# Kernel tuning notes

Hardware: AMD Instinct MI355X
Metric: run time of the kernel (lower is better)

Reference implementation:

```python
import jax, jax.numpy as jnp
import numpy as np

N, D_IN, D_OUT = 8192, 1024, 1024

def setup_inputs() -> dict:
    key = jax.random.key(0)
    k0, k1, k2, k3 = jax.random.split(key, 4)
    scale = 1.0 / np.sqrt(D_IN)
    return {
        "inputs": jax.random.normal(k0, (N, D_IN), dtype=jnp.float32),
        "W_q": jax.random.uniform(k1, (D_IN, D_OUT), jnp.float32, -scale, scale),
        "W_k": jax.random.uniform(k2, (D_IN, D_OUT), jnp.float32, -scale, scale),
        "W_v": jax.random.uniform(k3, (D_IN, D_OUT), jnp.float32, -scale, scale),
    }

def reference(inputs, W_q, W_k, W_v):
    # Linear projections (no bias): [N, d_out]
    q = inputs @ W_q
    k = inputs @ W_k
    v = inputs @ W_v
    d_k = k.shape[-1]
    # Full N x N scores, scaled softmax over last axis
    scores = (q @ k.T) / jnp.sqrt(jnp.asarray(d_k, q.dtype))
    attn = jax.nn.softmax(scores, axis=-1)
    return attn @ v
```

## Files before the change

kernel.cpp:

```cpp
#include <hip/hip_runtime.h>
#include <hip/hip_fp16.h>
#include <stdint.h>


typedef _Float16 half_t;
typedef _Float16 half8 __attribute__((ext_vector_type(8)));
typedef _Float16 half4 __attribute__((ext_vector_type(4)));
typedef float f32x4 __attribute__((ext_vector_type(4)));
typedef int i32x4 __attribute__((ext_vector_type(4)));

#define GLOAD16(gp, lp)                                                        \
  __builtin_amdgcn_global_load_lds(                                            \
      (__attribute__((address_space(1))) void*)(gp),                           \
      (__attribute__((address_space(3))) void*)(lp), 16, 0, 0)

#define BAR() __builtin_amdgcn_s_barrier()
#define LGKM0() asm volatile("s_waitcnt lgkmcnt(0)")
#define VMCNT8() asm volatile("s_waitcnt vmcnt(8)")
#define VMCNT4() asm volatile("s_waitcnt vmcnt(4)")
#define VMCNT0() asm volatile("s_waitcnt vmcnt(0)")

__global__ __launch_bounds__(256) void cast_f32_to_f16(
    const float* __restrict__ in, half_t* __restrict__ out, int n4) {
  int i = blockIdx.x * 256 + threadIdx.x;
  if (i < n4) {
    float4 v = ((const float4*)in)[i];
    half4 o = {(half_t)v.x, (half_t)v.y, (half_t)v.z, (half_t)v.w};
    ((half4*)out)[i] = o;
  }
}

template <typename Tin>
__global__ __launch_bounds__(256) void transpose_cast(
    const Tin* __restrict__ in, int ldin, half_t* __restrict__ out, int ldout,
    int R, int C) {
  __shared__ half_t tile[64][65];
  const int c0 = blockIdx.x * 64, r0 = blockIdx.y * 64;
  const int tx = threadIdx.x & 63, ty = threadIdx.x >> 6;
#pragma unroll
  for (int i = 0; i < 16; i++) {
    int r = ty * 16 + i;
    tile[r][tx] = (half_t)in[(size_t)(r0 + r) * ldin + c0 + tx];
  }
  __syncthreads();
#pragma unroll
  for (int i = 0; i < 16; i++) {
    int c = ty * 16 + i;
    out[(size_t)(c0 + c) * ldout + r0 + tx] = tile[tx][c];
  }
}

__global__ __launch_bounds__(256) void quant_i8(
    const half_t* __restrict__ in, int ldin, int8_t* __restrict__ out,
    int ldout, int n8) {
  int i = blockIdx.x * 256 + threadIdx.x;
  if (i >= n8) return;
  int row = i >> 7;
  int g = (i & 127) * 8;
  half8 v = *(const half8*)(in + (size_t)row * ldin + g);
  int b[8];
#pragma unroll
  for (int j = 0; j < 8; j++) {
    float f = (float)v[j] * 32.f;
    f = fminf(fmaxf(f, -127.f), 127.f);
    b[j] = (int)rintf(f);
  }
  int lo = (b[0] & 255) | ((b[1] & 255) << 8) | ((b[2] & 255) << 16) |
           ((b[3] & 255) << 24);
  int hi = (b[4] & 255) | ((b[5] & 255) << 8) | ((b[6] & 255) << 16) |
           ((b[7] & 255) << 24);
  int2* p = (int2*)(out + (size_t)row * ldout + g);
  *p = make_int2(lo, hi);
}

__global__ __launch_bounds__(256) void rowsum_recip(
    const float* __restrict__ rowpart, float* __restrict__ rinv, int rows,
    int w4) {
  int r = blockIdx.x * 256 + threadIdx.x;
  if (r < rows) {
    const float4* p = (const float4*)(rowpart + (size_t)r * (w4 * 4));
    float s = 0.f;
    for (int i = 0; i < w4; i++) {
      float4 v = p[i];
      s += v.x + v.y + v.z + v.w;
    }
    rinv[r] = 1.f / s;
  }
}

__global__ __launch_bounds__(256) void reduce_add2_norm(
    const float4* __restrict__ a, const float4* __restrict__ b,
    const float* __restrict__ rinv, float4* __restrict__ o, int n) {
  int i = blockIdx.x * 256 + threadIdx.x;
  if (i < n) {
    float4 x = a[i], y = b[i];
    float s = rinv[i >> 8];
    x.x = (x.x + y.x) * s;
    x.y = (x.y + y.y) * s;
    x.z = (x.z + y.z) * s;
    x.w = (x.w + y.w) * s;
    o[i] = x;
  }
}

template <typename To, int MODE>
__global__ __launch_bounds__(512, 2) void gemm256(
    const half_t* __restrict__ A, int lda, const half_t* __restrict__ Bt,
    int ldb, To* __restrict__ C, int ldc, int M, int N, int K, int ychunks,
    int SG, float* __restrict__ rowpart) {
  __shared__ __align__(16) char sm[131072];

  const int t = threadIdx.x;
  const int w = t >> 6;
  const int ln = t & 63;

  const int nwg = gridDim.x * gridDim.y;
  const int bid = blockIdx.y * gridDim.x + blockIdx.x;
  const int cpx = nwg >> 3;
  const int q = (bid & 7) * cpx + (bid >> 3);
  const int tiles_y = gridDim.y / ychunks;
  const int per_chunk = gridDim.x * tiles_y;
  const int chunk = q / per_chunk;
  int r_ = q - chunk * per_chunk;
  const int sw = SG * tiles_y;
  const int s_ = r_ / sw;
  r_ -= s_ * sw;
  const int by = r_ / SG;
  const int bx = s_ * SG + (r_ - by * SG);

  A += (size_t)chunk * K;
  Bt += (size_t)chunk * K;
  C += (size_t)chunk * M * ldc;

  const int row0 = by * 256;
  const int col0 = bx * 256;

  const int srow = w * 8 + (ln >> 3);
  const int sslot = (ln & 7) ^ ((ln >> 3) & 7);
  const half_t* Ag = A + (size_t)(row0 + srow) * lda + sslot * 8;
  const half_t* Bg = Bt + (size_t)(col0 + srow) * ldb + sslot * 8;
  const int ldsw = w * 1024;

#define STAGE_AB(kt, bb)                                                       \
  do {                                                                         \
    const half_t* ga_ = Ag + (size_t)(kt) * 64;                                \
    const half_t* gb_ = Bg + (size_t)(kt) * 64;                                \
    GLOAD16(ga_, sm + (bb) + ldsw);                                            \
    GLOAD16(ga_ + 64 * (size_t)lda, sm + (bb) + 8192 + ldsw);                  \
    GLOAD16(ga_ + 128 * (size_t)lda, sm + (bb) + 16384 + ldsw);                \
    GLOAD16(ga_ + 192 * (size_t)lda, sm + (bb) + 24576 + ldsw);                \
    GLOAD16(gb_, sm + (bb) + 32768 + ldsw);                                    \
    GLOAD16(gb_ + 64 * (size_t)ldb, sm + (bb) + 40960 + ldsw);                 \
    GLOAD16(gb_ + 128 * (size_t)ldb, sm + (bb) + 49152 + ldsw);                \
    GLOAD16(gb_ + 192 * (size_t)ldb, sm + (bb) + 57344 + ldsw);                \
  } while (0)

  const int wr = w >> 2;
  const int wc = w & 3;
  const int fr = ln & 15;
  const int kg = ln >> 4;
  const int sx0 = ((kg ^ (fr & 7)) << 4);
  const int sx1 = sx0 ^ 64;
  const int arow = (wr * 128 + fr) * 128;
  const int brow = 32768 + (wc * 64 + fr) * 128;

#define READ_A(MI0, cb)                                                        \
  _Pragma("unroll") for (int mi = 0; mi < 4; mi++) {                           \
    a4[mi][0] = *(const half8*)(sm + (cb) + arow + (MI0 + mi) * 2048 + sx0);   \
    a4[mi][1] = *(const half8*)(sm + (cb) + arow + (MI0 + mi) * 2048 + sx1);   \
  }
#define READ_B(NI, cb)                                                         \
  do {                                                                         \
    b8[NI][0] = *(const half8*)(sm + (cb) + brow + (NI) * 2048 + sx0);         \
    b8[NI][1] = *(const half8*)(sm + (cb) + brow + (NI) * 2048 + sx1);         \
  } while (0)

#define MFMA_Q(MI0, NI0)                                                       \
  __builtin_amdgcn_s_setprio(1);                                               \
  _Pragma("unroll") for (int kk = 0; kk < 2; kk++)                             \
  _Pragma("unroll") for (int mi = 0; mi < 4; mi++)                             \
  _Pragma("unroll") for (int ni = 0; ni < 2; ni++)                             \
      acc[MI0 + mi][NI0 + ni] = __builtin_amdgcn_mfma_f32_16x16x32_f16(        \
          a4[mi][kk], b8[NI0 + ni][kk], acc[MI0 + mi][NI0 + ni], 0, 0, 0);     \
  __builtin_amdgcn_s_setprio(0);

  half8 a4[4][2], b8[4][2];
  f32x4 acc[8][4] = {};

  const int NT = K >> 6;

  STAGE_AB(0, 0);
  STAGE_AB(1, 65536);
  VMCNT8();
  BAR();

#define TILE(tt, cb)                                                           \
  do {                                                                         \
    READ_A(0, cb);                                                             \
    READ_B(0, cb);                                                             \
    READ_B(1, cb);                                                             \
    BAR();                                                                     \
    LGKM0();                                                                   \
    MFMA_Q(0, 0);                                                              \
    BAR();                                                                     \
    READ_B(2, cb);                                                             \
    READ_B(3, cb);                                                             \
    BAR();                                                                     \
    LGKM0();                                                                   \
    MFMA_Q(0, 2);                                                              \
    BAR();                                                                     \
    READ_A(4, cb);                                                             \
    BAR();                                                                     \
    LGKM0();                                                                   \
    MFMA_Q(4, 2);                                                              \
    BAR();                                                                     \
    if ((tt) + 2 < NT) {                                                       \
      STAGE_AB((tt) + 2, cb);                                                  \
      VMCNT8();                                                                \
    } else {                                                                   \
      VMCNT0();                                                                \
    }                                                                          \
    BAR();                                                                     \
    MFMA_Q(4, 0);                                                              \
    BAR();                                                                     \
  } while (0)

  for (int kt = 0; kt < NT; kt += 2) {
    TILE(kt, 0);
    TILE(kt + 1, 65536);
  }

  const int orow = row0 + wr * 128 + (ln >> 4) * 4;
  const int ocol = col0 + wc * 64 + (ln & 15);
#pragma unroll
  for (int mi = 0; mi < 8; mi++)
#pragma unroll
    for (int ni = 0; ni < 4; ni++) {
      To* cp = C + (size_t)(orow + mi * 16) * ldc + ocol + ni * 16;
#pragma unroll
      for (int j = 0; j < 4; j++) cp[(size_t)j * ldc] = (To)acc[mi][ni][j];
    }
#undef TILE
#undef MFMA_Q
#undef READ_A
#undef READ_B
#undef STAGE_AB
}

__global__ __launch_bounds__(512, 2) void gemm256_i8exp(
    const int8_t* __restrict__ A, int lda, const int8_t* __restrict__ Bt,
    int ldb, half_t* __restrict__ C, int ldc, int K, int SG,
    float* __restrict__ rowpart) {
  __shared__ __align__(16) char sm[65536];

  const int t = threadIdx.x;
  const int w = t >> 6;
  const int ln = t & 63;

  const int nwg = gridDim.x * gridDim.y;
  const int bid = blockIdx.y * gridDim.x + blockIdx.x;
  const int cpx = nwg >> 3;
  const int q = (bid & 7) * cpx + (bid >> 3);
  const int sw = SG * gridDim.y;
  const int s_ = q / sw;
  int r_ = q - s_ * sw;
  const int by = r_ / SG;
  const int bx = s_ * SG + (r_ - by * SG);

  const int row0 = by * 256;
  const int col0 = bx * 256;

  const int rt = w * 16 + (ln >> 2);
  const int sl = (ln & 3) ^ ((rt >> 1) & 3);
  const int8_t* Ag = A + (size_t)(row0 + rt) * lda + sl * 16;
  const int8_t* Bg = Bt + (size_t)(col0 + rt) * ldb + sl * 16;
  const int ldsw = w * 1024;

#define STAGE8(kt, bb)                                                         \
  do {                                                                         \
    const int8_t* ga_ = Ag + (size_t)(kt) * 64;                                \
    const int8_t* gb_ = Bg + (size_t)(kt) * 64;                                \
    GLOAD16(ga_, sm + (bb) + ldsw);                                            \
    GLOAD16(ga_ + 128 * (size_t)lda, sm + (bb) + 8192 + ldsw);                 \
    GLOAD16(gb_, sm + (bb) + 16384 + ldsw);                                    \
    GLOAD16(gb_ + 128 * (size_t)ldb, sm + (bb) + 24576 + ldsw);                \
  } while (0)

  const int wr = w >> 2;
  const int wc = w & 3;
  const int fr = ln & 15;
  const int kg = ln >> 4;
  const int sx = (kg ^ ((fr >> 1) & 3)) << 4;
  const int arow = (wr * 128 + fr) * 64;
  const int brow = 16384 + (wc * 64 + fr) * 64;

#define READ_A8(MI0, cb)                                                       \
  _Pragma("unroll") for (int mi = 0; mi < 4; mi++)                             \
      a8[mi] = *(const i32x4*)(sm + (cb) + arow + (MI0 + mi) * 1024 + sx);
#define READ_B8(NI, cb)                                                        \
  b8v[NI] = *(const i32x4*)(sm + (cb) + brow + (NI) * 1024 + sx);

#define MFMA_Q8(MI0, NI0)                                                      \
  __builtin_amdgcn_s_setprio(1);                                               \
  _Pragma("unroll") for (int mi = 0; mi < 4; mi++)                             \
  _Pragma("unroll") for (int ni = 0; ni < 2; ni++)                             \
      acc[MI0 + mi][NI0 + ni] = __builtin_amdgcn_mfma_i32_16x16x64_i8(         \
          a8[mi], b8v[NI0 + ni], acc[MI0 + mi][NI0 + ni], 0, 0, 0);            \
  __builtin_amdgcn_s_setprio(0);

  i32x4 a8[4], b8v[4];
  i32x4 acc[8][4] = {};

  const int NT = K >> 6;

  STAGE8(0, 0);
  STAGE8(1, 32768);
  VMCNT4();
  BAR();

#define TILE8(tt, cb)                                                          \
  do {                                                                         \
    READ_A8(0, cb);                                                            \
    READ_B8(0, cb);                                                            \
    READ_B8(1, cb);                                                            \
    BAR();                                                                     \
    LGKM0();                                                                   \
    MFMA_Q8(0, 0);                                                             \
    BAR();                                                                     \
    READ_B8(2, cb);                                                            \
    READ_B8(3, cb);                                                            \
    BAR();                                                                     \
    LGKM0();                                                                   \
    MFMA_Q8(0, 2);                                                             \
    BAR();                                                                     \
    READ_A8(4, cb);                                                            \
    BAR();                                                                     \
    LGKM0();                                                                   \
    MFMA_Q8(4, 2);                                                             \
    BAR();                                                                     \
    if ((tt) + 2 < NT) {                                                       \
      STAGE8((tt) + 2, cb);                                                    \
      VMCNT4();                                                                \
    } else {                                                                   \
      VMCNT0();                                                                \
    }                                                                          \
    BAR();                                                                     \
    MFMA_Q8(4, 0);                                                             \
    BAR();                                                                     \
  } while (0)

  for (int kt = 0; kt < NT; kt += 2) {
    TILE8(kt, 0);
    TILE8(kt + 1, 32768);
  }

  const int orow = row0 + wr * 128 + (ln >> 4) * 4;
  const int ocol = col0 + wc * 64 + (ln & 15);
  const float sc = 3.0517578125e-5f;
  const int rp_ld = gridDim.x * 4;
#pragma unroll
  for (int mi = 0; mi < 8; mi++) {
#pragma unroll
    for (int j = 0; j < 4; j++) {
      const int r = orow + mi * 16 + j;
      float s = 0.f;
#pragma unroll
      for (int ni = 0; ni < 4; ni++) {
        float e = __expf((float)acc[mi][ni][j] * sc);
        C[(size_t)r * ldc + ocol + ni * 16] = (half_t)e;
        s += e;
      }
      s += __shfl_xor(s, 1);
      s += __shfl_xor(s, 2);
      s += __shfl_xor(s, 4);
      s += __shfl_xor(s, 8);
      if ((ln & 15) == 0) rowpart[(size_t)r * rp_ld + bx * 4 + wc] = s;
    }
  }
#undef TILE8
#undef MFMA_Q8
#undef READ_A8
#undef READ_B8
#undef STAGE8
}

extern "C" void kernel_launch(void* const* d_in, const int* in_sizes, int n_in,
                              void* d_out, int out_size, void* d_ws,
                              size_t ws_size, hipStream_t stream) {
  const float* X = (const float*)d_in[0];
  const float* Wq = (const float*)d_in[1];
  const float* Wk = (const float*)d_in[2];
  const float* Wv = (const float*)d_in[3];
  float* out = (float*)d_out;

  const int N = 8192, D = 1024;

  char* ws = (char*)d_ws;
  half_t* Xh  = (half_t*)(ws);
  half_t* Wth = (half_t*)(ws + (16ull << 20));
  half_t* QKV = (half_t*)(ws + (22ull << 20));
  half_t* Vt  = (half_t*)(ws + (70ull << 20));
  half_t* S   = (half_t*)(ws + (86ull << 20));
  float*  rowpart = (float*)ws;
  float*  rinv    = (float*)(ws + (4ull << 20));
  float*  part    = (float*)(ws + (5ull << 20));
  int8_t* Qi8     = (int8_t*)(ws + (6ull << 20));
  int8_t* Ki8     = (int8_t*)(ws + (14ull << 20));

  cast_f32_to_f16<<<(N * D / 4 + 255) / 256, 256, 0, stream>>>(X, Xh, N * D / 4);

  dim3 tg(D / 64, D / 64);
  transpose_cast<float><<<tg, 256, 0, stream>>>(Wq, D, Wth + 0ull * D * D, D, D, D);
  transpose_cast<float><<<tg, 256, 0, stream>>>(Wk, D, Wth + 1ull * D * D, D, D, D);
  transpose_cast<float><<<tg, 256, 0, stream>>>(Wv, D, Wth + 2ull * D * D, D, D, D);

  gemm256<half_t, 0><<<dim3(3 * D / 256, N / 256), 512, 0, stream>>>(
      Xh, D, Wth, D, QKV, 3 * D, N, 3 * D, D, 1, 4, nullptr);

  quant_i8<<<(N * 128 + 255) / 256, 256, 0, stream>>>(QKV, 3 * D, Qi8, D,
                                                      N * 128);
  quant_i8<<<(N * 128 + 255) / 256, 256, 0, stream>>>(QKV + D, 3 * D, Ki8, D,
                                                      N * 128);

  gemm256_i8exp<<<dim3(N / 256, N / 256), 512, 0, stream>>>(
      Qi8, D, Ki8, D, S, N, D, 8, rowpart);

  rowsum_recip<<<(N + 255) / 256, 256, 0, stream>>>(rowpart, rinv, N, 32);

  transpose_cast<half_t><<<dim3(D / 64, N / 64), 256, 0, stream>>>(
      QKV + 2 * D, 3 * D, Vt, N, N, D);

  gemm256<float, 0><<<dim3(D / 256, 2 * N / 256), 512, 0, stream>>>(
      S, N, Vt, N, part, D, N, D, N / 2, 2, 4, nullptr);

  reduce_add2_norm<<<(N * D / 4 + 255) / 256, 256, 0, stream>>>(
      (const float4*)part, (const float4*)(part + (size_t)N * D), rinv,
      (float4*)out, N * D / 4);
}
```

Measured before the change: 348.4 us.

## Fuse int8 quantization into QKV GEMM epilogue and cut barriers in int8 GEMM

The QKV projection GEMM now quantizes Q and K to int8 directly in its epilogue and writes only V in fp16, which removes the two quant_i8 kernels and the fp16 Q/K round trip. The PV GEMM applies the row-sum reciprocal in its epilogue and writes fp16 partials, and a lighter reduce kernel adds the two halves into the fp32 output, halving the partial traffic. The int8 QK GEMM drops several intra-tile barriers, issues all B reads together and overlaps the last MFMA quarter with the next stage load. Risks are byte-granular scattered int8 stores in the epilogue, extra fp16 rounding of partials, and LDS hazards from removing barriers.

```diff
diff --git a/kernel.cpp b/kernel.cpp
--- a/kernel.cpp
+++ b/kernel.cpp
@@ -48,29 +48,6 @@
     int c = ty * 16 + i;
     out[(size_t)(c0 + c) * ldout + r0 + tx] = tile[tx][c];
   }
-}
-
-__global__ __launch_bounds__(256) void quant_i8(
-    const half_t* __restrict__ in, int ldin, int8_t* __restrict__ out,
-    int ldout, int n8) {
-  int i = blockIdx.x * 256 + threadIdx.x;
-  if (i >= n8) return;
-  int row = i >> 7;
-  int g = (i & 127) * 8;
-  half8 v = *(const half8*)(in + (size_t)row * ldin + g);
-  int b[8];
-#pragma unroll
-  for (int j = 0; j < 8; j++) {
-    float f = (float)v[j] * 32.f;
-    f = fminf(fmaxf(f, -127.f), 127.f);
-    b[j] = (int)rintf(f);
-  }
-  int lo = (b[0] & 255) | ((b[1] & 255) << 8) | ((b[2] & 255) << 16) |
-           ((b[3] & 255) << 24);
-  int hi = (b[4] & 255) | ((b[5] & 255) << 8) | ((b[6] & 255) << 16) |
-           ((b[7] & 255) << 24);
-  int2* p = (int2*)(out + (size_t)row * ldout + g);
-  *p = make_int2(lo, hi);
 }
 
 __global__ __launch_bounds__(256) void rowsum_recip(
@@ -88,18 +65,23 @@
   }
 }
 
-__global__ __launch_bounds__(256) void reduce_add2_norm(
-    const float4* __restrict__ a, const float4* __restrict__ b,
-    const float* __restrict__ rinv, float4* __restrict__ o, int n) {
+__global__ __launch_bounds__(256) void reduce_add2h(
+    const half8* __restrict__ a, const half8* __restrict__ b,
+    float4* __restrict__ o, int n8) {
   int i = blockIdx.x * 256 + threadIdx.x;
-  if (i < n) {
-    float4 x = a[i], y = b[i];
-    float s = rinv[i >> 8];
-    x.x = (x.x + y.x) * s;
-    x.y = (x.y + y.y) * s;
-    x.z = (x.z + y.z) * s;
-    x.w = (x.w + y.w) * s;
-    o[i] = x;
+  if (i < n8) {
+    half8 x = a[i], y = b[i];
+    float4 o0, o1;
+    o0.x = (float)x[0] + (float)y[0];
+    o0.y = (float)x[1] + (float)y[1];
+    o0.z = (float)x[2] + (float)y[2];
+    o0.w = (float)x[3] + (float)y[3];
+    o1.x = (float)x[4] + (float)y[4];
+    o1.y = (float)x[5] + (float)y[5];
+    o1.z = (float)x[6] + (float)y[6];
+    o1.w = (float)x[7] + (float)y[7];
+    o[2 * i] = o0;
+    o[2 * i + 1] = o1;
   }
 }
 
@@ -107,7 +89,8 @@
 __global__ __launch_bounds__(512, 2) void gemm256(
     const half_t* __restrict__ A, int lda, const half_t* __restrict__ Bt,
     int ldb, To* __restrict__ C, int ldc, int M, int N, int K, int ychunks,
-    int SG, float* __restrict__ rowpart) {
+    int SG, const float* __restrict__ rinv, int8_t* __restrict__ qi8,
+    int8_t* __restrict__ ki8) {
   __shared__ __align__(16) char sm[131072];
 
   const int t = threadIdx.x;
@@ -232,14 +215,54 @@
 
   const int orow = row0 + wr * 128 + (ln >> 4) * 4;
   const int ocol = col0 + wc * 64 + (ln & 15);
-#pragma unroll
-  for (int mi = 0; mi < 8; mi++)
-#pragma unroll
-    for (int ni = 0; ni < 4; ni++) {
-      To* cp = C + (size_t)(orow + mi * 16) * ldc + ocol + ni * 16;
-#pragma unroll
-      for (int j = 0; j < 4; j++) cp[(size_t)j * ldc] = (To)acc[mi][ni][j];
+  if constexpr (MODE == 2) {
+    if (bx < 8) {
+      int8_t* qk = bx < 4 ? qi8 : ki8;
+      const int cbase = ocol - (bx < 4 ? 0 : 1024);
+#pragma unroll
+      for (int mi = 0; mi < 8; mi++)
+#pragma unroll
+        for (int j = 0; j < 4; j++) {
+          const size_t r = orow + mi * 16 + j;
+#pragma unroll
+          for (int ni = 0; ni < 4; ni++) {
+            float f = acc[mi][ni][j] * 32.f;
+            f = fminf(fmaxf(f, -127.f), 127.f);
+            qk[r * 1024 + cbase + ni * 16] = (int8_t)rintf(f);
+          }
+        }
+    } else {
+      const int cbase = ocol - 2048;
+#pragma unroll
+      for (int mi = 0; mi < 8; mi++)
+#pragma unroll
+        for (int ni = 0; ni < 4; ni++) {
+          To* cp = C + (size_t)(orow + mi * 16) * ldc + cbase + ni * 16;
+#pragma unroll
+          for (int j = 0; j < 4; j++) cp[(size_t)j * ldc] = (To)acc[mi][ni][j];
+        }
     }
+  } else if constexpr (MODE == 3) {
+#pragma unroll
+    for (int mi = 0; mi < 8; mi++)
+#pragma unroll
+      for (int j = 0; j < 4; j++) {
+        const size_t r = orow + mi * 16 + j;
+        const float s = rinv[r];
+#pragma unroll
+        for (int ni = 0; ni < 4; ni++)
+          C[r * ldc + ocol + ni * 16] = (To)(acc[mi][ni][j] * s);
+      }
+  } else {
+#pragma unroll
+    for (int mi = 0; mi < 8; mi++)
+#pragma unroll
+      for (int ni = 0; ni < 4; ni++) {
+        To* cp = C + (size_t)(orow + mi * 16) * ldc + ocol + ni * 16;
+#pragma unroll
+        for (int j = 0; j < 4; j++) cp[(size_t)j * ldc] = (To)acc[mi][ni][j];
+      }
+  }
 #undef TILE
 #undef MFMA_Q
 #undef READ_A
@@ -320,33 +343,29 @@
 
 #define TILE8(tt, cb)                                                          \
   do {                                                                         \
+                                                                       \
     READ_A8(0, cb);                                                            \
     READ_B8(0, cb);                                                            \
     READ_B8(1, cb);                                                            \
-    BAR();                                                                     \
+    READ_B8(2, cb);                                                            \
+    READ_B8(3, cb);                                                            \
     LGKM0();                                                                   \
     MFMA_Q8(0, 0);                                                             \
-    BAR();                                                                     \
-    READ_B8(2, cb);                                                            \
-    READ_B8(3, cb);                                                            \
-    BAR();                                                                     \
-    LGKM0();                                                                   \
     MFMA_Q8(0, 2);                                                             \
-    BAR();                                                                     \
+                                                                       \
     READ_A8(4, cb);                                                            \
-    BAR();                                                                     \
     LGKM0();                                                                   \
     MFMA_Q8(4, 2);                                                             \
-    BAR();                                                                     \
+    BAR();     \
     if ((tt) + 2 < NT) {                                                       \
       STAGE8((tt) + 2, cb);                                                    \
-      VMCNT4();                                                                \
+      MFMA_Q8(4, 0);                                                           \
+      VMCNT4();                     \
     } else {                                                                   \
+      MFMA_Q8(4, 0);                                                           \
       VMCNT0();                                                                \
     }                                                                          \
-    BAR();                                                                     \
-    MFMA_Q8(4, 0);                                                             \
-    BAR();                                                                     \
+    BAR();                             \
   } while (0)
 
   for (int kt = 0; kt < NT; kt += 2) {
@@ -396,16 +415,16 @@
   const int N = 8192, D = 1024;
 
   char* ws = (char*)d_ws;
-  half_t* Xh  = (half_t*)(ws);
-  half_t* Wth = (half_t*)(ws + (16ull << 20));
-  half_t* QKV = (half_t*)(ws + (22ull << 20));
-  half_t* Vt  = (half_t*)(ws + (70ull << 20));
-  half_t* S   = (half_t*)(ws + (86ull << 20));
-  float*  rowpart = (float*)ws;
-  float*  rinv    = (float*)(ws + (4ull << 20));
-  float*  part    = (float*)(ws + (5ull << 20));
-  int8_t* Qi8     = (int8_t*)(ws + (6ull << 20));
-  int8_t* Ki8     = (int8_t*)(ws + (14ull << 20));
+  half_t* Xh   = (half_t*)(ws);
+  half_t* Wth  = (half_t*)(ws + (16ull << 20));
+  half_t* Vh   = (half_t*)(ws + (22ull << 20));
+  half_t* partH= (half_t*)(ws + (38ull << 20));
+  int8_t* Qi8  = (int8_t*)(ws + (70ull << 20));
+  int8_t* Ki8  = (int8_t*)(ws + (78ull << 20));
+  half_t* Vt   = (half_t*)(ws + (70ull << 20));
+  half_t* S    = (half_t*)(ws + (86ull << 20));
+  float* rowpart = (float*)ws;
+  float* rinv    = (float*)(ws + (4ull << 20));
 
   cast_f32_to_f16<<<(N * D / 4 + 255) / 256, 256, 0, stream>>>(X, Xh, N * D / 4);
 
@@ -414,13 +433,8 @@
   transpose_cast<float><<<tg, 256, 0, stream>>>(Wk, D, Wth + 1ull * D * D, D, D, D);
   transpose_cast<float><<<tg, 256, 0, stream>>>(Wv, D, Wth + 2ull * D * D, D, D, D);
 
-  gemm256<half_t, 0><<<dim3(3 * D / 256, N / 256), 512, 0, stream>>>(
-      Xh, D, Wth, D, QKV, 3 * D, N, 3 * D, D, 1, 4, nullptr);
-
-  quant_i8<<<(N * 128 + 255) / 256, 256, 0, stream>>>(QKV, 3 * D, Qi8, D,
-                                                      N * 128);
-  quant_i8<<<(N * 128 + 255) / 256, 256, 0, stream>>>(QKV + D, 3 * D, Ki8, D,
-                                                      N * 128);
+  gemm256<half_t, 2><<<dim3(3 * D / 256, N / 256), 512, 0, stream>>>(
+      Xh, D, Wth, D, Vh, D, N, 3 * D, D, 1, 4, nullptr, Qi8, Ki8);
 
   gemm256_i8exp<<<dim3(N / 256, N / 256), 512, 0, stream>>>(
       Qi8, D, Ki8, D, S, N, D, 8, rowpart);
@@ -428,12 +442,12 @@
   rowsum_recip<<<(N + 255) / 256, 256, 0, stream>>>(rowpart, rinv, N, 32);
 
   transpose_cast<half_t><<<dim3(D / 64, N / 64), 256, 0, stream>>>(
-      QKV + 2 * D, 3 * D, Vt, N, N, D);
-
-  gemm256<float, 0><<<dim3(D / 256, 2 * N / 256), 512, 0, stream>>>(
-      S, N, Vt, N, part, D, N, D, N / 2, 2, 4, nullptr);
-
-  reduce_add2_norm<<<(N * D / 4 + 255) / 256, 256, 0, stream>>>(
-      (const float4*)part, (const float4*)(part + (size_t)N * D), rinv,
-      (float4*)out, N * D / 4);
-}
+      Vh, D, Vt, N, N, D);
+
+  gemm256<half_t, 3><<<dim3(D / 256, 2 * N / 256), 512, 0, stream>>>(
+      S, N, Vt, N, partH, D, N, D, N / 2, 2, 4, rinv, nullptr, nullptr);
+
+  reduce_add2h<<<(N * D / 8 + 255) / 256, 256, 0, stream>>>(
+      (const half8*)partH, (const half8*)(partH + (size_t)N * D), (float4*)out,
+      N * D / 8);
+}
```

Result: faster. 323.9 us (-7.0%).
